# Kernel optimization log

Hardware: AMD Instinct MI355X
Metric: run time of the kernel (lower is better)

## Reference

```python
import jax, jax.numpy as jnp
import numpy as np

H, E, R = 1024, 48, 32  # hidden size, num entities, num relation types
MAX_START = 200


def setup_inputs() -> dict:
    key = jax.random.key(0)
    ks = jax.random.split(key, 6)
    return {
        "entity_emb": jax.random.normal(ks[0], (E, H), jnp.float32),
        "rel_emb": jax.random.normal(ks[1], (R, H), jnp.float32),
        "W1": jax.random.normal(ks[2], (3 * H, H), jnp.float32) / np.sqrt(3 * H).astype(np.float32),
        "b1": jnp.zeros((H,), jnp.float32),
        "W2": jax.random.normal(ks[3], (H, 1), jnp.float32) / np.sqrt(H).astype(np.float32),
        "b2": jnp.zeros((1,), jnp.float32),
        "entity_starts": jax.random.randint(ks[4], (E,), 0, MAX_START, jnp.int32),
        "max_distance": 50,
    }


def reference(entity_emb, rel_emb, W1, b1, W2, b2, entity_starts, max_distance):
    """Vectorized equivalent of the triple loop: for every (subj i, obj j, rel k)
    score = sigmoid(MLP(cat([subj, rel, obj]))), masked by i != j and
    |start_i - start_j| <= max_distance. Dropout is identity at eval."""
    e, h = entity_emb.shape
    r = rel_emb.shape[0]
    # build all triplet inputs [E, E, R, 3H] (cat order: subject, relation, object)
    s = jnp.broadcast_to(entity_emb[:, None, None, :], (e, e, r, h))
    rel = jnp.broadcast_to(rel_emb[None, None, :, :], (e, e, r, h))
    o = jnp.broadcast_to(entity_emb[None, :, None, :], (e, e, r, h))
    trip = jnp.concatenate([s, rel, o], axis=-1)  # [E, E, R, 3H]
    hid = jax.nn.relu(jnp.einsum("sorf,fh->sorh", trip, W1) + b1)  # [E, E, R, H]
    logits = jnp.einsum("sorh,hx->sorx", hid, W2)[..., 0] + b2[0]  # [E, E, R]
    scores = jax.nn.sigmoid(logits)
    # pair mask: no self-relations, distance cutoff
    dist = jnp.abs(entity_starts[:, None] - entity_starts[None, :])
    mask = (dist <= max_distance) & (~jnp.eye(e, dtype=bool))  # [E, E]
    return jnp.where(mask[:, :, None], scores, jnp.zeros((), scores.dtype))
```

## Files before the change

### kernel.cpp

```cpp
#include <hip/hip_runtime.h>
#include <hip/hip_bf16.h>
#include <math.h>

#define Hh 1024
#define Ee 48
#define Rr 32
#define PITCH_A 1028
#define GP_A 1028
#define BKa 256
#define PITCH_B 260
#define CH_B 256

union F4 { float4 v; float f[4]; };

__global__ __launch_bounds__(512) void kA_table(const float* __restrict__ ent,
                                                const float* __restrict__ rel,
                                                const float* __restrict__ W1,
                                                const float* __restrict__ b1,
                                                float* __restrict__ T) {
    __shared__ float emb_s[16 * PITCH_A];
    __shared__ float w_s[2][8 * GP_A];
    const int tid = threadIdx.x;
    const int rt = blockIdx.x & 7;
    const int h0 = (blockIdx.x >> 3) * 32;
    const int row0 = rt * 16;

    const float* emb; int foff;
    if (row0 < 48)      { emb = ent + row0 * Hh;        foff = 0;      }
    else if (row0 < 80) { emb = rel + (row0 - 48) * Hh; foff = Hh;     }
    else                { emb = ent + (row0 - 80) * Hh; foff = 2 * Hh; }

    for (int q = 0; q < 8; ++q) {
        const int id4 = tid + q * 512;
        const int r = id4 >> 8, o4 = id4 & 255;
        *reinterpret_cast<float4*>(&emb_s[r * PITCH_A + o4 * 4]) =
            *reinterpret_cast<const float4*>(&emb[r * Hh + o4 * 4]);
    }

    const int w    = tid >> 6;
    const int lane = tid & 63;
    const int h4g  = lane & 7;
    const int rsub = lane >> 3;
    const int r0 = rsub * 2;

    const int sc4 = tid & 7;
    const int sfb = tid >> 3;
    auto stage = [&](int buf, int c) {
        const float* gp = &W1[(size_t)(foff + c * BKa + sfb) * Hh + h0 + sc4 * 4];
        float4 v0 = *reinterpret_cast<const float4*>(gp);
        float4 v1 = *reinterpret_cast<const float4*>(gp + (size_t)64 * Hh);
        float4 v2 = *reinterpret_cast<const float4*>(gp + (size_t)128 * Hh);
        float4 v3 = *reinterpret_cast<const float4*>(gp + (size_t)192 * Hh);
        float* lp = &w_s[buf][sc4 * GP_A + sfb * 4];
        *reinterpret_cast<float4*>(lp)       = v0;
        *reinterpret_cast<float4*>(lp + 256) = v1;
        *reinterpret_cast<float4*>(lp + 512) = v2;
        *reinterpret_cast<float4*>(lp + 768) = v3;
    };

    stage(0, 0);
    __syncthreads();

    float acc0[4] = {0.f, 0.f, 0.f, 0.f};
    float acc1[4] = {0.f, 0.f, 0.f, 0.f};

    for (int c = 0; c < 4; ++c) {
        if (c < 3) stage((c + 1) & 1, c + 1);

        const float* wp  = &w_s[c & 1][h4g * GP_A + (w * 32) * 4];
        const float* e0p = &emb_s[r0 * PITCH_A + c * BKa + w * 32];
        const float* e1p = e0p + PITCH_A;

#pragma unroll
        for (int s = 0; s < 8; ++s) {
            F4 e0, e1;
            e0.v = *reinterpret_cast<const float4*>(e0p + s * 4);
            e1.v = *reinterpret_cast<const float4*>(e1p + s * 4);
#pragma unroll
            for (int ff = 0; ff < 4; ++ff) {
                F4 wv;
                wv.v = *reinterpret_cast<const float4*>(wp + (s * 4 + ff) * 4);
#pragma unroll
                for (int hh = 0; hh < 4; ++hh) {
                    acc0[hh] = fmaf(e0.f[ff], wv.f[hh], acc0[hh]);
                    acc1[hh] = fmaf(e1.f[ff], wv.f[hh], acc1[hh]);
                }
            }
        }
        __syncthreads();
    }

    {
        const int base = (w * 64 + lane) * 8;
        F4 o0, o1;
#pragma unroll
        for (int c = 0; c < 4; ++c) { o0.f[c] = acc0[c]; o1.f[c] = acc1[c]; }
        *reinterpret_cast<float4*>(&emb_s[base])     = o0.v;
        *reinterpret_cast<float4*>(&emb_s[base + 4]) = o1.v;
    }
    __syncthreads();
    {
        const int r = tid >> 5, h = tid & 31;
        const int src = ((r >> 1) * 8 + (h >> 2)) * 8 + (r & 1) * 4 + (h & 3);
        float s = 0.f;
#pragma unroll
        for (int ww = 0; ww < 8; ++ww) s += emb_s[ww * 512 + src];
        const int row = row0 + r;
        if (row >= 48 && row < 80) s += b1[h0 + h];
        T[row * Hh + h0 + h] = s;
    }
}

__global__ __launch_bounds__(512) void kB_triplets(const float* __restrict__ T,
                                                   const float* __restrict__ W2,
                                                   const float* __restrict__ b2,
                                                   const int* __restrict__ starts,
                                                   const int* __restrict__ maxd,
                                                   float* __restrict__ out) {
    __shared__ float se[2][42 * PITCH_B];
    const int tid = threadIdx.x;
    const int i  = blockIdx.x >> 2;
    const int js = (blockIdx.x >> 1) & 1;
    const int ks = blockIdx.x & 1;
    const int j0 = js * 24;
    const int k0 = ks * 16;

    const int w    = tid >> 6;
    const int lane = tid & 63;
    const int jG = lane & 7;
    const int kG = lane >> 3;

    auto stage = [&](int buf, int c) {
        const int hbase = c * CH_B;
        float4 v0, v1, v2, v3, v4, v5;
        int a5 = -1;
#define SRC_OF(ID4, VV)                                                       \
        {                                                                     \
            const int g = (ID4) >> 6, o4 = (ID4) & 63;                        \
            const float* src;                                                 \
            if (g == 41) src = W2 + hbase + o4 * 4;                           \
            else {                                                            \
                int grow;                                                     \
                if (g == 0)       grow = i;                                   \
                else if (g < 17)  grow = 48 + k0 + (g - 1);                   \
                else              grow = 80 + j0 + (g - 17);                  \
                src = T + grow * Hh + hbase + o4 * 4;                         \
            }                                                                 \
            VV = *reinterpret_cast<const float4*>(src);                       \
        }
        SRC_OF(tid,          v0)
        SRC_OF(tid + 512,    v1)
        SRC_OF(tid + 1024,   v2)
        SRC_OF(tid + 1536,   v3)
        SRC_OF(tid + 2048,   v4)
        if (tid < 128) { SRC_OF(tid + 2560, v5) a5 = tid + 2560; }
#undef SRC_OF
        float* b = se[buf];
        {
            const int id4 = tid;        *reinterpret_cast<float4*>(&b[(id4 >> 6) * PITCH_B + (id4 & 63) * 4]) = v0;
        }
        { const int id4 = tid + 512;    *reinterpret_cast<float4*>(&b[(id4 >> 6) * PITCH_B + (id4 & 63) * 4]) = v1; }
        { const int id4 = tid + 1024;   *reinterpret_cast<float4*>(&b[(id4 >> 6) * PITCH_B + (id4 & 63) * 4]) = v2; }
        { const int id4 = tid + 1536;   *reinterpret_cast<float4*>(&b[(id4 >> 6) * PITCH_B + (id4 & 63) * 4]) = v3; }
        { const int id4 = tid + 2048;   *reinterpret_cast<float4*>(&b[(id4 >> 6) * PITCH_B + (id4 & 63) * 4]) = v4; }
        if (a5 >= 0) { *reinterpret_cast<float4*>(&b[(a5 >> 6) * PITCH_B + (a5 & 63) * 4]) = v5; }
    };

    stage(0, 0);
    __syncthreads();

    float acc[3][2];
#pragma unroll
    for (int a = 0; a < 3; ++a) { acc[a][0] = 0.f; acc[a][1] = 0.f; }

    for (int c = 0; c < 4; ++c) {
        if (c < 3) stage((c + 1) & 1, c + 1);

        const float* sm = se[c & 1];
        const int hw = w * 32;
        const float* pa = sm + hw;
        const float* pw = sm + 41 * PITCH_B + hw;

#pragma unroll
        for (int s = 0; s < 8; ++s) {
            const int h4 = s * 4;
            F4 av, wv, rv[2], bv[3];
            av.v = *reinterpret_cast<const float4*>(pa + h4);
            wv.v = *reinterpret_cast<const float4*>(pw + h4);
#pragma unroll
            for (int tk = 0; tk < 2; ++tk)
                rv[tk].v = *reinterpret_cast<const float4*>(sm + (1 + kG + 8 * tk) * PITCH_B + hw + h4);
#pragma unroll
            for (int tj = 0; tj < 3; ++tj)
                bv[tj].v = *reinterpret_cast<const float4*>(sm + (17 + jG + 8 * tj) * PITCH_B + hw + h4);

#pragma unroll
            for (int cc = 0; cc < 4; ++cc) {
                const float a = av.f[cc], w2v = wv.f[cc];
                const float p0 = a + rv[0].f[cc];
                const float p1 = a + rv[1].f[cc];
#pragma unroll
                for (int tj = 0; tj < 3; ++tj) {
                    const float bb = bv[tj].f[cc];
                    float v0 = p0 + bb; v0 = v0 > 0.f ? v0 : 0.f;
                    acc[tj][0] = fmaf(v0, w2v, acc[tj][0]);
                    float v1 = p1 + bb; v1 = v1 > 0.f ? v1 : 0.f;
                    acc[tj][1] = fmaf(v1, w2v, acc[tj][1]);
                }
            }
        }
        __syncthreads();
    }

#pragma unroll
    for (int tj = 0; tj < 3; ++tj)
#pragma unroll
        for (int tk = 0; tk < 2; ++tk)
            se[0][w * 384 + (tj * 8 + jG) * 16 + tk * 8 + kG] = acc[tj][tk];
    __syncthreads();
    if (tid < 384) {
        float s = b2[0];
#pragma unroll
        for (int ww = 0; ww < 8; ++ww) s += se[0][ww * 384 + tid];
        const int jl = tid >> 4, kl = tid & 15;
        const int j = j0 + jl, k = k0 + kl;
        const float sc = 1.f / (1.f + expf(-s));
        int di = starts[i] - starts[j]; if (di < 0) di = -di;
        const bool m = (i != j) && (di <= maxd[0]);
        out[(i * Ee + j) * Rr + k] = m ? sc : 0.f;
    }
}

extern "C" void kernel_launch(void* const* d_in, const int* in_sizes, int n_in,
                              void* d_out, int out_size, void* d_ws, size_t ws_size,
                              hipStream_t stream) {
    const float* ent    = (const float*)d_in[0];
    const float* rel    = (const float*)d_in[1];
    const float* W1     = (const float*)d_in[2];
    const float* b1     = (const float*)d_in[3];
    const float* W2     = (const float*)d_in[4];
    const float* b2     = (const float*)d_in[5];
    const int*   starts = (const int*)d_in[6];
    const int*   maxd   = (const int*)d_in[7];
    float* out = (float*)d_out;

    float* T = (float*)d_ws;

    kA_table<<<256, 512, 0, stream>>>(ent, rel, W1, b1, T);
    kB_triplets<<<192, 512, 0, stream>>>(T, W2, b2, starts, maxd, out);
}
```

Before: 28.53 us.

## Fuse table and triplet kernels into one launch with a flag-based grid barrier

Merges the two kernels into a single persistent launch of 256 blocks. Each block first computes its slice of the projection table, then publishes a per-block flag. Block 0 waits on all 256 flags and raises a global release flag, and the other 191 blocks spin on that flag before running the triplet scoring phase. This removes the second launch and the gap between kernels, at the cost of spin-waiting. It assumes all 256 blocks are co-resident and that the flag sentinel values from earlier calls do not collide with the expected ones across repeated invocations.

```diff
diff --git a/kernel.cpp b/kernel.cpp
--- a/kernel.cpp
+++ b/kernel.cpp
@@ -12,6 +12,261 @@
 #define CH_B 256
 
 union F4 { float4 v; float f[4]; };
+
+__device__ __forceinline__ unsigned sent(int x) { return 0x9E3779B9u * (unsigned)(x + 1); }
+
+__global__ __launch_bounds__(512) void fused2(
+    const float* __restrict__ ent, const float* __restrict__ rel,
+    const float* __restrict__ W1, const float* __restrict__ b1,
+    const float* __restrict__ W2, const float* __restrict__ b2,
+    const int* __restrict__ starts, const int* __restrict__ maxd,
+    float* __restrict__ T, unsigned* __restrict__ flags,
+    float* __restrict__ out)
+{
+    __shared__ float smem[32896];
+    const int tid = threadIdx.x;
+    const int b = blockIdx.x;
+
+    float* emb_s = smem;
+    float* wsA   = smem + 16448;
+    float* wsB   = smem + 24672;
+
+    {
+        const int rt = b & 7;
+        const int h0 = (b >> 3) * 32;
+        const int row0 = rt * 16;
+
+        const float* emb; int foff;
+        if (row0 < 48)      { emb = ent + row0 * Hh;        foff = 0;      }
+        else if (row0 < 80) { emb = rel + (row0 - 48) * Hh; foff = Hh;     }
+        else                { emb = ent + (row0 - 80) * Hh; foff = 2 * Hh; }
+
+        for (int q = 0; q < 8; ++q) {
+            const int id4 = tid + q * 512;
+            const int r = id4 >> 8, o4 = id4 & 255;
+            *reinterpret_cast<float4*>(&emb_s[r * PITCH_A + o4 * 4]) =
+                *reinterpret_cast<const float4*>(&emb[r * Hh + o4 * 4]);
+        }
+
+        const int w    = tid >> 6;
+        const int lane = tid & 63;
+        const int h4g  = lane & 7;
+        const int rsub = lane >> 3;
+        const int r0 = rsub * 2;
+        const int sc4 = tid & 7;
+        const int sfb = tid >> 3;
+
+        auto stageA = [&](float* lb, int c) {
+            const float* gp = &W1[(size_t)(foff + c * BKa + sfb) * Hh + h0 + sc4 * 4];
+            float4 v0 = *reinterpret_cast<const float4*>(gp);
+            float4 v1 = *reinterpret_cast<const float4*>(gp + (size_t)64 * Hh);
+            float4 v2 = *reinterpret_cast<const float4*>(gp + (size_t)128 * Hh);
+            float4 v3 = *reinterpret_cast<const float4*>(gp + (size_t)192 * Hh);
+            float* lp = &lb[sc4 * GP_A + sfb * 4];
+            *reinterpret_cast<float4*>(lp)       = v0;
+            *reinterpret_cast<float4*>(lp + 256) = v1;
+            *reinterpret_cast<float4*>(lp + 512) = v2;
+            *reinterpret_cast<float4*>(lp + 768) = v3;
+        };
+
+        stageA(wsA, 0);
+        __syncthreads();
+
+        float acc0[4] = {0.f, 0.f, 0.f, 0.f};
+        float acc1[4] = {0.f, 0.f, 0.f, 0.f};
+
+        for (int c = 0; c < 4; ++c) {
+            const float* cur = (c & 1) ? wsB : wsA;
+            float* nxt       = (c & 1) ? wsA : wsB;
+            if (c < 3) stageA(nxt, c + 1);
+
+            const float* wp  = &cur[h4g * GP_A + (w * 32) * 4];
+            const float* e0p = &emb_s[r0 * PITCH_A + c * BKa + w * 32];
+            const float* e1p = e0p + PITCH_A;
+
+#pragma unroll
+            for (int s = 0; s < 8; ++s) {
+                F4 e0, e1;
+                e0.v = *reinterpret_cast<const float4*>(e0p + s * 4);
+                e1.v = *reinterpret_cast<const float4*>(e1p + s * 4);
+#pragma unroll
+                for (int ff = 0; ff < 4; ++ff) {
+                    F4 wv;
+                    wv.v = *reinterpret_cast<const float4*>(wp + (s * 4 + ff) * 4);
+#pragma unroll
+                    for (int hh = 0; hh < 4; ++hh) {
+                        acc0[hh] = fmaf(e0.f[ff], wv.f[hh], acc0[hh]);
+                        acc1[hh] = fmaf(e1.f[ff], wv.f[hh], acc1[hh]);
+                    }
+                }
+            }
+            __syncthreads();
+        }
+
+        {
+            const int base = (w * 64 + lane) * 8;
+            F4 o0, o1;
+#pragma unroll
+            for (int c = 0; c < 4; ++c) { o0.f[c] = acc0[c]; o1.f[c] = acc1[c]; }
+            *reinterpret_cast<float4*>(&emb_s[base])     = o0.v;
+            *reinterpret_cast<float4*>(&emb_s[base + 4]) = o1.v;
+        }
+        __syncthreads();
+        {
+            const int r = tid >> 5, h = tid & 31;
+            const int src = ((r >> 1) * 8 + (h >> 2)) * 8 + (r & 1) * 4 + (h & 3);
+            float s = 0.f;
+#pragma unroll
+            for (int ww = 0; ww < 8; ++ww) s += emb_s[ww * 512 + src];
+            const int row = row0 + r;
+            if (row >= 48 && row < 80) s += b1[h0 + h];
+            T[row * Hh + h0 + h] = s;
+        }
+    }
+
+    __threadfence();
+    __syncthreads();
+    if (tid == 0)
+        __hip_atomic_store(&flags[b], sent(b), __ATOMIC_RELEASE, __HIP_MEMORY_SCOPE_AGENT);
+    if (b >= 192) return;
+
+    if (b == 0) {
+        if (tid < 16) {
+            for (int q = 0; q < 16; ++q) {
+                const int f = tid * 16 + q;
+                const unsigned ev = sent(f);
+                while (__hip_atomic_load(&flags[f], __ATOMIC_ACQUIRE,
+                                         __HIP_MEMORY_SCOPE_AGENT) != ev)
+                    __builtin_amdgcn_s_sleep(4);
+            }
+        }
+        __syncthreads();
+        if (tid == 0)
+            __hip_atomic_store(&flags[256], sent(1000), __ATOMIC_RELEASE,
+                               __HIP_MEMORY_SCOPE_AGENT);
+    } else {
+        if (tid == 0) {
+            const unsigned ev = sent(1000);
+            while (__hip_atomic_load(&flags[256], __ATOMIC_ACQUIRE,
+                                     __HIP_MEMORY_SCOPE_AGENT) != ev)
+                __builtin_amdgcn_s_sleep(8);
+        }
+        __syncthreads();
+    }
+
+    {
+        float* pb0 = smem;
+        float* pb1 = smem + 10920;
+        const int i  = b >> 2;
+        const int js = (b >> 1) & 1;
+        const int ks = b & 1;
+        const int j0 = js * 24;
+        const int k0 = ks * 16;
+
+        const int w    = tid >> 6;
+        const int lane = tid & 63;
+        const int jG = lane & 7;
+        const int kG = lane >> 3;
+
+        auto stageB = [&](float* bb, int c) {
+            const int hbase = c * CH_B;
+            float4 v0, v1, v2, v3, v4, v5;
+            int a5 = -1;
+#define SRC_OF(ID4, VV)                                                       \
+            {                                                                 \
+                const int g = (ID4) >> 6, o4 = (ID4) & 63;                    \
+                const float* src;                                             \
+                if (g == 41) src = W2 + hbase + o4 * 4;                       \
+                else {                                                        \
+                    int grow;                                                 \
+                    if (g == 0)       grow = i;                               \
+                    else if (g < 17)  grow = 48 + k0 + (g - 1);               \
+                    else              grow = 80 + j0 + (g - 17);              \
+                    src = T + grow * Hh + hbase + o4 * 4;                     \
+                }                                                             \
+                VV = *reinterpret_cast<const float4*>(src);                   \
+            }
+            SRC_OF(tid,        v0)
+            SRC_OF(tid + 512,  v1)
+            SRC_OF(tid + 1024, v2)
+            SRC_OF(tid + 1536, v3)
+            SRC_OF(tid + 2048, v4)
+            if (tid < 128) { SRC_OF(tid + 2560, v5) a5 = tid + 2560; }
+#undef SRC_OF
+            { const int id4 = tid;        *reinterpret_cast<float4*>(&bb[(id4 >> 6) * PITCH_B + (id4 & 63) * 4]) = v0; }
+            { const int id4 = tid + 512;  *reinterpret_cast<float4*>(&bb[(id4 >> 6) * PITCH_B + (id4 & 63) * 4]) = v1; }
+            { const int id4 = tid + 1024; *reinterpret_cast<float4*>(&bb[(id4 >> 6) * PITCH_B + (id4 & 63) * 4]) = v2; }
+            { const int id4 = tid + 1536; *reinterpret_cast<float4*>(&bb[(id4 >> 6) * PITCH_B + (id4 & 63) * 4]) = v3; }
+            { const int id4 = tid + 2048; *reinterpret_cast<float4*>(&bb[(id4 >> 6) * PITCH_B + (id4 & 63) * 4]) = v4; }
+            if (a5 >= 0) { *reinterpret_cast<float4*>(&bb[(a5 >> 6) * PITCH_B + (a5 & 63) * 4]) = v5; }
+        };
+
+        stageB(pb0, 0);
+        __syncthreads();
+
+        float acc[3][2];
+#pragma unroll
+        for (int a = 0; a < 3; ++a) { acc[a][0] = 0.f; acc[a][1] = 0.f; }
+
+        for (int c = 0; c < 4; ++c) {
+            const float* sm = (c & 1) ? pb1 : pb0;
+            float* nb       = (c & 1) ? pb0 : pb1;
+            if (c < 3) stageB(nb, c + 1);
+
+            const int hw = w * 32;
+            const float* pa = sm + hw;
+            const float* pw = sm + 41 * PITCH_B + hw;
+
+#pragma unroll
+            for (int s = 0; s < 8; ++s) {
+                const int h4 = s * 4;
+                F4 av, wv, rv[2], bv[3];
+                av.v = *reinterpret_cast<const float4*>(pa + h4);
+                wv.v = *reinterpret_cast<const float4*>(pw + h4);
+#pragma unroll
+                for (int tk = 0; tk < 2; ++tk)
+                    rv[tk].v = *reinterpret_cast<const float4*>(sm + (1 + kG + 8 * tk) * PITCH_B + hw + h4);
+#pragma unroll
+                for (int tj = 0; tj < 3; ++tj)
+                    bv[tj].v = *reinterpret_cast<const float4*>(sm + (17 + jG + 8 * tj) * PITCH_B + hw + h4);
+
+#pragma unroll
+                for (int cc = 0; cc < 4; ++cc) {
+                    const float a = av.f[cc], w2v = wv.f[cc];
+                    const float p0 = a + rv[0].f[cc];
+                    const float p1 = a + rv[1].f[cc];
+#pragma unroll
+                    for (int tj = 0; tj < 3; ++tj) {
+                        const float bb = bv[tj].f[cc];
+                        float v0 = p0 + bb; v0 = v0 > 0.f ? v0 : 0.f;
+                        acc[tj][0] = fmaf(v0, w2v, acc[tj][0]);
+                        float v1 = p1 + bb; v1 = v1 > 0.f ? v1 : 0.f;
+                        acc[tj][1] = fmaf(v1, w2v, acc[tj][1]);
+                    }
+                }
+            }
+            __syncthreads();
+        }
+
+#pragma unroll
+        for (int tj = 0; tj < 3; ++tj)
+#pragma unroll
+            for (int tk = 0; tk < 2; ++tk)
+                pb0[w * 384 + (tj * 8 + jG) * 16 + tk * 8 + kG] = acc[tj][tk];
+        __syncthreads();
+        if (tid < 384) {
+            float s = b2[0];
+#pragma unroll
+            for (int ww = 0; ww < 8; ++ww) s += pb0[ww * 384 + tid];
+            const int jl = tid >> 4, kl = tid & 15;
+            const int j = j0 + jl, k = k0 + kl;
+            const float sc = 1.f / (1.f + expf(-s));
+            int di = starts[i] - starts[j]; if (di < 0) di = -di;
+            const bool m = (i != j) && (di <= maxd[0]);
+            out[(i * Ee + j) * Rr + k] = m ? sc : 0.f;
+        }
+    }
+}
 
 __global__ __launch_bounds__(512) void kA_table(const float* __restrict__ ent,
                                                 const float* __restrict__ rel,
@@ -42,7 +297,6 @@
     const int h4g  = lane & 7;
     const int rsub = lane >> 3;
     const int r0 = rsub * 2;
-
     const int sc4 = tid & 7;
     const int sfb = tid >> 3;
     auto stage = [&](int buf, int c) {
@@ -66,11 +320,9 @@
 
     for (int c = 0; c < 4; ++c) {
         if (c < 3) stage((c + 1) & 1, c + 1);
-
         const float* wp  = &w_s[c & 1][h4g * GP_A + (w * 32) * 4];
         const float* e0p = &emb_s[r0 * PITCH_A + c * BKa + w * 32];
         const float* e1p = e0p + PITCH_A;
-
 #pragma unroll
         for (int s = 0; s < 8; ++s) {
             F4 e0, e1;
@@ -124,7 +376,6 @@
     const int ks = blockIdx.x & 1;
     const int j0 = js * 24;
     const int k0 = ks * 16;
-
     const int w    = tid >> 6;
     const int lane = tid & 63;
     const int jG = lane & 7;
@@ -148,22 +399,20 @@
             }                                                                 \
             VV = *reinterpret_cast<const float4*>(src);                       \
         }
-        SRC_OF(tid,          v0)
-        SRC_OF(tid + 512,    v1)
-        SRC_OF(tid + 1024,   v2)
-        SRC_OF(tid + 1536,   v3)
-        SRC_OF(tid + 2048,   v4)
+        SRC_OF(tid,        v0)
+        SRC_OF(tid + 512,  v1)
+        SRC_OF(tid + 1024, v2)
+        SRC_OF(tid + 1536, v3)
+        SRC_OF(tid + 2048, v4)
         if (tid < 128) { SRC_OF(tid + 2560, v5) a5 = tid + 2560; }
 #undef SRC_OF
-        float* b = se[buf];
-        {
-            const int id4 = tid;        *reinterpret_cast<float4*>(&b[(id4 >> 6) * PITCH_B + (id4 & 63) * 4]) = v0;
-        }
-        { const int id4 = tid + 512;    *reinterpret_cast<float4*>(&b[(id4 >> 6) * PITCH_B + (id4 & 63) * 4]) = v1; }
-        { const int id4 = tid + 1024;   *reinterpret_cast<float4*>(&b[(id4 >> 6) * PITCH_B + (id4 & 63) * 4]) = v2; }
-        { const int id4 = tid + 1536;   *reinterpret_cast<float4*>(&b[(id4 >> 6) * PITCH_B + (id4 & 63) * 4]) = v3; }
-        { const int id4 = tid + 2048;   *reinterpret_cast<float4*>(&b[(id4 >> 6) * PITCH_B + (id4 & 63) * 4]) = v4; }
-        if (a5 >= 0) { *reinterpret_cast<float4*>(&b[(a5 >> 6) * PITCH_B + (a5 & 63) * 4]) = v5; }
+        float* bb = se[buf];
+        { const int id4 = tid;        *reinterpret_cast<float4*>(&bb[(id4 >> 6) * PITCH_B + (id4 & 63) * 4]) = v0; }
+        { const int id4 = tid + 512;  *reinterpret_cast<float4*>(&bb[(id4 >> 6) * PITCH_B + (id4 & 63) * 4]) = v1; }
+        { const int id4 = tid + 1024; *reinterpret_cast<float4*>(&bb[(id4 >> 6) * PITCH_B + (id4 & 63) * 4]) = v2; }
+        { const int id4 = tid + 1536; *reinterpret_cast<float4*>(&bb[(id4 >> 6) * PITCH_B + (id4 & 63) * 4]) = v3; }
+        { const int id4 = tid + 2048; *reinterpret_cast<float4*>(&bb[(id4 >> 6) * PITCH_B + (id4 & 63) * 4]) = v4; }
+        if (a5 >= 0) { *reinterpret_cast<float4*>(&bb[(a5 >> 6) * PITCH_B + (a5 & 63) * 4]) = v5; }
     };
 
     stage(0, 0);
@@ -175,12 +424,10 @@
 
     for (int c = 0; c < 4; ++c) {
         if (c < 3) stage((c + 1) & 1, c + 1);
-
         const float* sm = se[c & 1];
         const int hw = w * 32;
         const float* pa = sm + hw;
         const float* pw = sm + 41 * PITCH_B + hw;
-
 #pragma unroll
         for (int s = 0; s < 8; ++s) {
             const int h4 = s * 4;
@@ -193,7 +440,6 @@
 #pragma unroll
             for (int tj = 0; tj < 3; ++tj)
                 bv[tj].v = *reinterpret_cast<const float4*>(sm + (17 + jG + 8 * tj) * PITCH_B + hw + h4);
-
 #pragma unroll
             for (int cc = 0; cc < 4; ++cc) {
                 const float a = av.f[cc], w2v = wv.f[cc];
@@ -243,9 +489,16 @@
     const int*   starts = (const int*)d_in[6];
     const int*   maxd   = (const int*)d_in[7];
     float* out = (float*)d_out;
-
-    float* T = (float*)d_ws;
-
-    kA_table<<<256, 512, 0, stream>>>(ent, rel, W1, b1, T);
-    kB_triplets<<<192, 512, 0, stream>>>(T, W2, b2, starts, maxd, out);
+    char* ws = (char*)d_ws;
+
+    float* T = (float*)ws;
+    unsigned* flags = (unsigned*)(ws + ((size_t)1 << 20));
+
+    if (ws_size >= ((size_t)1 << 20) + 4096) {
+        fused2<<<256, 512, 0, stream>>>(ent, rel, W1, b1, W2, b2, starts, maxd,
+                                        T, flags, out);
+    } else {
+        kA_table<<<256, 512, 0, stream>>>(ent, rel, W1, b1, T);
+        kB_triplets<<<192, 512, 0, stream>>>(T, W2, b2, starts, maxd, out);
+    }
 }
```

After: 65.12 us. 128% more time.
